# Optimization experiments

Measured on AMD Instinct MI355X. Metric: run time of the kernel, lower is better.

The kernel has to match this reference:

```python
import jax, jax.numpy as jnp
import numpy as np

H = 16      # numHeads (== numKeyValueHeads since keyValueHeadsPerHead=1)
D = 128     # headDim


def setup_inputs() -> dict:
    key = jax.random.key(0)
    k1, k2, k3 = jax.random.split(key, 3)
    B, S, dim = 2, 2048, 2048
    x = jax.random.normal(k1, (B, S, dim), dtype=jnp.float32)
    # qkvProj: Linear(dim -> (H + 2*H)*D) without bias; torch Linear weight is [out, in]
    Wqkv = jax.random.normal(k2, ((H + 2 * H) * D, dim), dtype=jnp.float32) * 0.02
    # outProj: Linear(H*D -> dim) without bias
    Wout = jax.random.normal(k3, (dim, H * D), dtype=jnp.float32) * 0.02
    return {"x": x, "Wqkv": Wqkv, "Wout": Wout}


def reference(x, Wqkv, Wout):
    B, S, _ = x.shape
    qkv = jnp.einsum('bsd,ed->bse', x, Wqkv)           # [B, S, 3*H*D]
    qkv = qkv.reshape(B, S, 3 * H, D)
    q = qkv[:, :, :H]                                  # [B, S, H, D]
    k = qkv[:, :, H:2 * H]                             # [B, S, H, D]
    v = qkv[:, :, 2 * H:]                              # [B, S, H, D]
    # explicit QK^T / sqrt(d), softmax in fp32, then @ V (keyValueHeadsPerHead=1
    # collapses the group axis, leaving standard per-head attention)
    logits = jnp.einsum('bqhd,bkhd->bhqk', q, k) * (D ** -0.5)
    w = jax.nn.softmax(logits.astype(jnp.float32), axis=-1).astype(logits.dtype)
    out = jnp.einsum('bhqk,bkhd->bqhd', w, v).reshape(B, S, H * D)
    return jnp.einsum('bse,de->bsd', out, Wout)        # outProj
```

## Files before the change

kernel.cpp:

```cpp
#include <hip/hip_runtime.h>

typedef __bf16 bf16x8 __attribute__((ext_vector_type(8)));
typedef _Float16 f16;
typedef f16 f16x8 __attribute__((ext_vector_type(8)));
typedef float f32x4 __attribute__((ext_vector_type(4)));
typedef unsigned short u16;
typedef u16 u16x4 __attribute__((ext_vector_type(4)));

__device__ __forceinline__ u16 f2bf(float f) {
  unsigned u = __builtin_bit_cast(unsigned, f);
  u += 0x7FFFu + ((u >> 16) & 1u);
  return (u16)(u >> 16);
}

#define GLDS16(g, l) __builtin_amdgcn_global_load_lds(                     \
    (const __attribute__((address_space(1))) unsigned int*)(g),            \
    (__attribute__((address_space(3))) unsigned int*)(l), 16, 0, 0)

__device__ __forceinline__ f32x4 mfma16(bf16x8 a, bf16x8 b, f32x4 c) {
  return __builtin_amdgcn_mfma_f32_16x16x32_bf16(a, b, c, 0, 0, 0);
}
__device__ __forceinline__ f32x4 mfma16h(f16x8 a, f16x8 b, f32x4 c) {
  return __builtin_amdgcn_mfma_f32_16x16x32_f16(a, b, c, 0, 0, 0);
}

__global__ void cvt_bf16(const float* __restrict__ src, u16* __restrict__ dst,
                         int n4, int n4s, float scale) {
  int idx = blockIdx.x * blockDim.x + threadIdx.x;
  int stride = gridDim.x * blockDim.x;
  for (int i = idx; i < n4; i += stride) {
    float4 v = ((const float4*)src)[i];
    float sc = (i < n4s) ? scale : 1.0f;
    u16x4 o = { f2bf(v.x * sc), f2bf(v.y * sc), f2bf(v.z * sc), f2bf(v.w * sc) };
    ((u16x4*)dst)[i] = o;
  }
}

template<int MODE>
__global__ __launch_bounds__(256, 3) void gemm_bt(
    const u16* __restrict__ A, const u16* __restrict__ B,
    void* __restrict__ C, u16* __restrict__ VT,
    int M, int N, int K) {
  __shared__ __align__(16) u16 As[2][128 * 32];
  __shared__ __align__(16) u16 Bs[2][128 * 32];
  const int t = threadIdx.x;
  const int lane = t & 63;
  const int w = t >> 6;
  const int wm = w >> 1, wn = w & 1;
  const int l15 = lane & 15, lg = lane >> 4;
  const int m0 = blockIdx.y * 128, n0 = blockIdx.x * 128;
  f32x4 acc[4][4] = {};

  const int srow = t >> 2;
  const int schunk = (t & 3) ^ ((srow >> 1) & 3);
  const u16* ga = A + (size_t)(m0 + srow) * K + schunk * 8;
  const u16* gb = B + (size_t)(n0 + srow) * K + schunk * 8;
  const size_t half = (size_t)64 * K;
  const int ro = l15 * 32 + ((lg ^ ((l15 >> 1) & 3)) * 8);

#define STG(kt, bf) do {                                                   \
    const int ko_ = (kt) * 32;                                             \
    GLDS16(ga + ko_,        &As[bf][0] + t * 8);                           \
    GLDS16(ga + half + ko_, &As[bf][2048] + t * 8);                        \
    GLDS16(gb + ko_,        &Bs[bf][0] + t * 8);                           \
    GLDS16(gb + half + ko_, &Bs[bf][2048] + t * 8);                        \
  } while (0)

#define BODY(bf) do {                                                      \
    const u16* la_ = &As[bf][0];                                           \
    const u16* lb_ = &Bs[bf][0];                                           \
    bf16x8 af[4], bfr[4];                                                  \
    _Pragma("unroll")                                                      \
    for (int i_ = 0; i_ < 4; ++i_)                                         \
      af[i_] = *(const bf16x8*)&la_[(wm * 64 + i_ * 16) * 32 + ro];        \
    _Pragma("unroll")                                                      \
    for (int i_ = 0; i_ < 4; ++i_)                                         \
      bfr[i_] = *(const bf16x8*)&lb_[(wn * 64 + i_ * 16) * 32 + ro];       \
    __builtin_amdgcn_s_setprio(1);                                         \
    _Pragma("unroll")                                                      \
    for (int i_ = 0; i_ < 4; ++i_)                                         \
      _Pragma("unroll")                                                    \
      for (int j_ = 0; j_ < 4; ++j_)                                       \
        acc[i_][j_] = mfma16(af[i_], bfr[j_], acc[i_][j_]);                \
    __builtin_amdgcn_s_setprio(0);                                         \
  } while (0)

  const int NT = K / 32;
  STG(0, 0);
#pragma unroll 1
  for (int T = 0; T < NT - 1; ++T) {
    STG(T + 1, (T + 1) & 1);
    asm volatile("s_waitcnt vmcnt(4)" ::: "memory");
    __builtin_amdgcn_sched_barrier(0);
    __builtin_amdgcn_s_barrier();
    __builtin_amdgcn_sched_barrier(0);
    BODY(T & 1);
    asm volatile("s_waitcnt lgkmcnt(0)" ::: "memory");
    __builtin_amdgcn_sched_barrier(0);
    __builtin_amdgcn_s_barrier();
    __builtin_amdgcn_sched_barrier(0);
  }
  asm volatile("s_waitcnt vmcnt(0)" ::: "memory");
  __builtin_amdgcn_sched_barrier(0);
  __builtin_amdgcn_s_barrier();
  __builtin_amdgcn_sched_barrier(0);
  BODY((NT - 1) & 1);
#undef STG
#undef BODY

  const int rbase = m0 + wm * 64 + (lg << 2);
  const int cbase = n0 + wn * 64 + l15;
#pragma unroll
  for (int i = 0; i < 4; ++i) {
#pragma unroll
    for (int j = 0; j < 4; ++j) {
      const int row0 = rbase + i * 16;
      const int col = cbase + j * 16;
      if (MODE == 0) {
        if (col < 4096) {
          u16* cq = (u16*)C;
#pragma unroll
          for (int jj = 0; jj < 4; ++jj)
            cq[(size_t)(row0 + jj) * 4096 + col] = f2bf(acc[i][j][jj]);
        } else {
          const int bb = row0 >> 11, s = row0 & 2047;
          auto h0 = __builtin_amdgcn_cvt_pkrtz(acc[i][j][0], acc[i][j][1]);
          auto h1 = __builtin_amdgcn_cvt_pkrtz(acc[i][j][2], acc[i][j][3]);
          uint2 pk;
          pk.x = __builtin_bit_cast(unsigned, h0);
          pk.y = __builtin_bit_cast(unsigned, h1);
          *(uint2*)&VT[(size_t)(bb * 2048 + (col - 4096)) * 2048 + s] = pk;
        }
      } else {
        float* cf = (float*)C;
#pragma unroll
        for (int jj = 0; jj < 4; ++jj)
          cf[(size_t)(row0 + jj) * N + col] = acc[i][j][jj];
      }
    }
  }
}

#define PSTRIDE 72
__global__ __launch_bounds__(512, 1) void attn_fwd(
    const u16* __restrict__ qk, const u16* __restrict__ vt, u16* __restrict__ aout) {
  __shared__ __align__(16) u16 Ks[2][64 * 128];
  __shared__ __align__(16) u16 Vs[2][128 * 64];
  __shared__ __align__(16) u16 Pl[8][32 * PSTRIDE];
  const int t = threadIdx.x, lane = t & 63, w = t >> 6;
  const int bh = blockIdx.x;
  const int b = bh >> 4, h = bh & 15;
  const int q0 = blockIdx.y * 256 + w * 32;
  const int l15 = lane & 15, lg = lane >> 4;

  const u16* qp = qk + (size_t)b * 2048 * 4096 + h * 128;
  const u16* kp = qp + 2048;
  const u16* vtp = vt + (size_t)(b * 16 + h) * 128 * 2048;
  u16* op = aout + (size_t)b * 2048 * 2048 + h * 128;

  int ksoff[2], vsoff[2];
#pragma unroll
  for (int rd = 0; rd < 2; ++rd) {
    const int r = rd * 32 + (t >> 4);
    const int c = (t & 15) ^ (r & 15);
    ksoff[rd] = r * 4096 + c * 8;
    const int rv = rd * 64 + (t >> 3);
    const int cv = (t & 7) ^ (rv & 7);
    vsoff[rd] = rv * 2048 + cv * 8;
  }

  bf16x8 qf[2][4];
#pragma unroll
  for (int mi = 0; mi < 2; ++mi)
#pragma unroll
    for (int kd = 0; kd < 4; ++kd)
      qf[mi][kd] = *(const bf16x8*)&qp[(size_t)(q0 + mi * 16 + l15) * 4096 + kd * 32 + lg * 8];

  f32x4 o[2][8] = {};
  f32x4 lacc[2] = {};
  const f16x8 onesf = {f16(1.f), f16(1.f), f16(1.f), f16(1.f),
                       f16(1.f), f16(1.f), f16(1.f), f16(1.f)};
  u16* pw = &Pl[w][0];

#pragma unroll
  for (int rd = 0; rd < 2; ++rd) {
    GLDS16(kp + ksoff[rd], &Ks[0][0] + rd * 4096 + t * 8);
    GLDS16(vtp + vsoff[rd], &Vs[0][0] + rd * 4096 + t * 8);
  }
  __syncthreads();

  auto tile = [&](const u16* ksb, const u16* vsb, u16* kpre, u16* vpre, int nextit) {
    if (nextit < 32) {
      const size_t kt1 = (size_t)nextit * 64;
#pragma unroll
      for (int rd = 0; rd < 2; ++rd) {
        GLDS16(kp + kt1 * 4096 + ksoff[rd], kpre + rd * 4096 + t * 8);
        GLDS16(vtp + kt1 + vsoff[rd], vpre + rd * 4096 + t * 8);
      }
    }
    f32x4 sf[2][4];
    __builtin_amdgcn_s_setprio(1);
#pragma unroll
    for (int ni = 0; ni < 4; ++ni) {
      const int r = ni * 16 + l15;
      bf16x8 kf[4];
#pragma unroll
      for (int kd = 0; kd < 4; ++kd)
        kf[kd] = *(const bf16x8*)&ksb[r * 128 + (((kd * 4 + lg) ^ l15) * 8)];
#pragma unroll
      for (int mi = 0; mi < 2; ++mi) {
        f32x4 s = {0.f, 0.f, 0.f, 0.f};
        s = mfma16(kf[0], qf[mi][0], s);
        s = mfma16(kf[1], qf[mi][1], s);
        s = mfma16(kf[2], qf[mi][2], s);
        s = mfma16(kf[3], qf[mi][3], s);
        sf[mi][ni] = s;
      }
    }
    __builtin_amdgcn_s_setprio(0);

#pragma unroll
    for (int mi = 0; mi < 2; ++mi)
#pragma unroll
      for (int ni = 0; ni < 4; ++ni) {
        float p0 = exp2f(sf[mi][ni][0]);
        float p1 = exp2f(sf[mi][ni][1]);
        float p2 = exp2f(sf[mi][ni][2]);
        float p3 = exp2f(sf[mi][ni][3]);
        auto h0 = __builtin_amdgcn_cvt_pkrtz(p0, p1);
        auto h1 = __builtin_amdgcn_cvt_pkrtz(p2, p3);
        uint2 wv;
        wv.x = __builtin_bit_cast(unsigned, h0);
        wv.y = __builtin_bit_cast(unsigned, h1);
        *(uint2*)&pw[(mi * 16 + l15) * PSTRIDE + ni * 16 + lg * 4] = wv;
      }

    f16x8 pa[2][2];
#pragma unroll
    for (int mi = 0; mi < 2; ++mi)
#pragma unroll
      for (int ks = 0; ks < 2; ++ks)
        pa[mi][ks] = *(const f16x8*)&pw[(mi * 16 + l15) * PSTRIDE + ks * 32 + lg * 8];
    __builtin_amdgcn_s_setprio(1);
#pragma unroll
    for (int mi = 0; mi < 2; ++mi) {
      lacc[mi] = mfma16h(pa[mi][0], onesf, lacc[mi]);
      lacc[mi] = mfma16h(pa[mi][1], onesf, lacc[mi]);
    }
#pragma unroll
    for (int n2 = 0; n2 < 8; ++n2) {
      const int r = n2 * 16 + l15;
      f16x8 vf0 = *(const f16x8*)&vsb[r * 64 + (((0 * 4 + lg) ^ (l15 & 7)) * 8)];
      f16x8 vf1 = *(const f16x8*)&vsb[r * 64 + (((1 * 4 + lg) ^ (l15 & 7)) * 8)];
#pragma unroll
      for (int mi = 0; mi < 2; ++mi) {
        o[mi][n2] = mfma16h(pa[mi][0], vf0, o[mi][n2]);
        o[mi][n2] = mfma16h(pa[mi][1], vf1, o[mi][n2]);
      }
    }
    __builtin_amdgcn_s_setprio(0);
    __syncthreads();
  };

#pragma unroll 1
  for (int it = 0; it < 32; it += 2) {
    tile(&Ks[0][0], &Vs[0][0], &Ks[1][0], &Vs[1][0], it + 1);
    tile(&Ks[1][0], &Vs[1][0], &Ks[0][0], &Vs[0][0], it + 2);
  }

#pragma unroll
  for (int mi = 0; mi < 2; ++mi)
#pragma unroll
    for (int j = 0; j < 4; ++j) {
      float inv = 1.f / lacc[mi][j];
#pragma unroll
      for (int n2 = 0; n2 < 8; ++n2)
        op[(size_t)(q0 + mi * 16 + lg * 4 + j) * 2048 + n2 * 16 + l15] =
            f2bf(o[mi][n2][j] * inv);
    }
}

extern "C" void kernel_launch(void* const* d_in, const int* in_sizes, int n_in,
                              void* d_out, int out_size, void* d_ws, size_t ws_size,
                              hipStream_t stream) {
  const float* x    = (const float*)d_in[0];
  const float* Wqkv = (const float*)d_in[1];
  const float* Wout = (const float*)d_in[2];
  float* out = (float*)d_out;

  u16* ws = (u16*)d_ws;
  u16* xb    = ws;
  u16* wqkvb = ws + 8388608;
  u16* woutb = ws + 20971520;
  u16* qkbuf = ws + 25165824;
  u16* vtbuf = ws + 41943040;
  u16* aout  = xb;

  const float qscale = 0.08838834764831845f * 1.4426950408889634f;

  cvt_bf16<<<2048, 256, 0, stream>>>(x,    xb,    8388608 / 4, 0, 1.0f);
  cvt_bf16<<<2048, 256, 0, stream>>>(Wqkv, wqkvb, 12582912 / 4, 4194304 / 4, qscale);
  cvt_bf16<<<1024, 256, 0, stream>>>(Wout, woutb, 4194304 / 4, 0, 1.0f);

  gemm_bt<0><<<dim3(48, 32), 256, 0, stream>>>(xb, wqkvb, (void*)qkbuf, vtbuf,
                                               4096, 6144, 2048);
  attn_fwd<<<dim3(32, 8, 1), 512, 0, stream>>>(qkbuf, vtbuf, aout);
  gemm_bt<1><<<dim3(16, 32), 256, 0, stream>>>(aout, woutb, (void*)out, nullptr,
                                               4096, 2048, 2048);
}
```

Baseline: 277.0 us.

## Add dedicated QKV GEMM kernel with 128x192 tiles and direct-register A loads; read V from global in attention

Replaces the generic QKV projection GEMM with a specialized kernel. It uses 128x192 output tiles, a 64-wide K step, and an XCD-aware block remapping. The A operand is loaded straight into registers from global memory with a one-step lookahead, and only B is staged through LDS. Separately, the attention kernel stops staging V^T through LDS and reads V fragments directly from global memory each tile. This frees LDS and drops the V staging loads, but V reads become uncoalesced global loads in the inner loop and may stall the MFMA pipeline.

```diff
diff --git a/kernel.cpp b/kernel.cpp
--- a/kernel.cpp
+++ b/kernel.cpp
@@ -36,11 +36,124 @@
   }
 }
 
-template<int MODE>
+__global__ __launch_bounds__(256, 2) void gemm1_qkv(
+    const u16* __restrict__ A, const u16* __restrict__ B,
+    u16* __restrict__ QK, u16* __restrict__ VT) {
+  __shared__ __align__(16) u16 LB[2][12288];
+  constexpr int K = 2048;
+  const int t = threadIdx.x, lane = t & 63, w = t >> 6;
+  const int wm = w >> 1, wn = w & 1;
+  const int l15 = lane & 15, lg = lane >> 4;
+  const int l7 = l15 & 7;
+
+  const int bid = blockIdx.x;
+  const int wg = (bid & 7) * 128 + (bid >> 3);
+  const int bx = wg & 31, by = wg >> 5;
+  const int m0 = by * 128, n0 = bx * 192;
+
+  const int srow = t >> 3;
+  const int schunk = (t & 7) ^ (srow & 7);
+  const u16* gb = B + (size_t)(n0 + srow) * K + schunk * 8;
+
+  const u16* gaf = A + (size_t)(m0 + wm * 64 + l15) * K + lg * 8;
+
+  f32x4 acc[4][6] = {};
+  bf16x8 aC[2][4], aN[2][4];
+
+#define STG_B6(kt, bfi) do {                                               \
+    GLDS16(gb + (kt) * 64 + (size_t)0 * 32 * K, &LB[bfi][0]     + t * 8);  \
+    GLDS16(gb + (kt) * 64 + (size_t)1 * 32 * K, &LB[bfi][2048]  + t * 8);  \
+    GLDS16(gb + (kt) * 64 + (size_t)2 * 32 * K, &LB[bfi][4096]  + t * 8);  \
+    GLDS16(gb + (kt) * 64 + (size_t)3 * 32 * K, &LB[bfi][6144]  + t * 8);  \
+    GLDS16(gb + (kt) * 64 + (size_t)4 * 32 * K, &LB[bfi][8192]  + t * 8);  \
+    GLDS16(gb + (kt) * 64 + (size_t)5 * 32 * K, &LB[bfi][10240] + t * 8);  \
+  } while (0)
+
+#define ITER(AC, AN, P, TT) do {                                           \
+    const bool st_ = (TT) < 31;                                            \
+    asm volatile("s_waitcnt lgkmcnt(0)" ::: "memory");                     \
+    __builtin_amdgcn_s_barrier();                                          \
+    if (st_) {                                                             \
+      _Pragma("unroll")                                                    \
+      for (int kk = 0; kk < 2; ++kk)                                       \
+        _Pragma("unroll")                                                  \
+        for (int i = 0; i < 4; ++i)                                        \
+          AN[kk][i] = *(const bf16x8*)&gaf[(size_t)i * 16 * K +            \
+                                           ((TT) + 1) * 64 + kk * 32];     \
+      STG_B6((TT) + 1, (P) ^ 1);                                           \
+      asm volatile("s_waitcnt vmcnt(14)" ::: "memory");                    \
+    } else {                                                               \
+      asm volatile("s_waitcnt vmcnt(0)" ::: "memory");                     \
+    }                                                                      \
+    __builtin_amdgcn_s_barrier();                                          \
+    const u16* lb_ = &LB[P][0];                                            \
+    bf16x8 bLo[2][3], bHi[2][3];                                           \
+    _Pragma("unroll")                                                      \
+    for (int kk = 0; kk < 2; ++kk) {                                       \
+      const int cp_ = ((kk * 4 + lg) ^ l7) * 8;                            \
+      _Pragma("unroll")                                                    \
+      for (int j = 0; j < 3; ++j) {                                        \
+        bLo[kk][j] = *(const bf16x8*)&lb_[(wn * 96 + j * 16 + l15) * 64 + cp_]; \
+        bHi[kk][j] = *(const bf16x8*)&lb_[(wn * 96 + 48 + j * 16 + l15) * 64 + cp_]; \
+      }                                                                    \
+    }                                                                      \
+    __builtin_amdgcn_s_setprio(1);                                         \
+    _Pragma("unroll")                                                      \
+    for (int i = 0; i < 4; ++i)                                            \
+      _Pragma("unroll")                                                    \
+      for (int j = 0; j < 6; ++j)                                          \
+        _Pragma("unroll")                                                  \
+        for (int kk = 0; kk < 2; ++kk)                                     \
+          acc[i][j] = mfma16(AC[kk][i],                                    \
+                             (j < 3 ? bLo[kk][j] : bHi[kk][j - 3]),        \
+                             acc[i][j]);                                   \
+    __builtin_amdgcn_s_setprio(0);                                         \
+  } while (0)
+
+#pragma unroll
+  for (int kk = 0; kk < 2; ++kk)
+#pragma unroll
+    for (int i = 0; i < 4; ++i)
+      aC[kk][i] = *(const bf16x8*)&gaf[(size_t)i * 16 * K + kk * 32];
+  STG_B6(0, 0);
+
+#pragma unroll 1
+  for (int T = 0; T < 32; T += 2) {
+    ITER(aC, aN, 0, T);
+    ITER(aN, aC, 1, T + 1);
+  }
+#undef STG_B6
+#undef ITER
+
+  const int rb = m0 + wm * 64 + lg * 4;
+  const int cb = n0 + wn * 96 + l15;
+#pragma unroll
+  for (int i = 0; i < 4; ++i) {
+#pragma unroll
+    for (int j = 0; j < 6; ++j) {
+      const int row0 = rb + i * 16;
+      const int col = cb + j * 16;
+      if (col < 4096) {
+#pragma unroll
+        for (int jj = 0; jj < 4; ++jj)
+          QK[(size_t)(row0 + jj) * 4096 + col] = f2bf(acc[i][j][jj]);
+      } else {
+        const int vcol = col - 4096;
+        const int bb = row0 >> 11, s = row0 & 2047;
+        auto h0 = __builtin_amdgcn_cvt_pkrtz(acc[i][j][0], acc[i][j][1]);
+        auto h1 = __builtin_amdgcn_cvt_pkrtz(acc[i][j][2], acc[i][j][3]);
+        uint2 pk;
+        pk.x = __builtin_bit_cast(unsigned, h0);
+        pk.y = __builtin_bit_cast(unsigned, h1);
+        *(uint2*)&VT[((size_t)bb * 2048 + vcol) * 2048 + s] = pk;
+      }
+    }
+  }
+}
+
 __global__ __launch_bounds__(256, 3) void gemm_bt(
     const u16* __restrict__ A, const u16* __restrict__ B,
-    void* __restrict__ C, u16* __restrict__ VT,
-    int M, int N, int K) {
+    float* __restrict__ C, int M, int N, int K) {
   __shared__ __align__(16) u16 As[2][128 * 32];
   __shared__ __align__(16) u16 Bs[2][128 * 32];
   const int t = threadIdx.x;
@@ -111,41 +224,21 @@
   const int rbase = m0 + wm * 64 + (lg << 2);
   const int cbase = n0 + wn * 64 + l15;
 #pragma unroll
-  for (int i = 0; i < 4; ++i) {
+  for (int i = 0; i < 4; ++i)
 #pragma unroll
     for (int j = 0; j < 4; ++j) {
       const int row0 = rbase + i * 16;
       const int col = cbase + j * 16;
-      if (MODE == 0) {
-        if (col < 4096) {
-          u16* cq = (u16*)C;
-#pragma unroll
-          for (int jj = 0; jj < 4; ++jj)
-            cq[(size_t)(row0 + jj) * 4096 + col] = f2bf(acc[i][j][jj]);
-        } else {
-          const int bb = row0 >> 11, s = row0 & 2047;
-          auto h0 = __builtin_amdgcn_cvt_pkrtz(acc[i][j][0], acc[i][j][1]);
-          auto h1 = __builtin_amdgcn_cvt_pkrtz(acc[i][j][2], acc[i][j][3]);
-          uint2 pk;
-          pk.x = __builtin_bit_cast(unsigned, h0);
-          pk.y = __builtin_bit_cast(unsigned, h1);
-          *(uint2*)&VT[(size_t)(bb * 2048 + (col - 4096)) * 2048 + s] = pk;
-        }
-      } else {
-        float* cf = (float*)C;
-#pragma unroll
-        for (int jj = 0; jj < 4; ++jj)
-          cf[(size_t)(row0 + jj) * N + col] = acc[i][j][jj];
-      }
-    }
-  }
+#pragma unroll
+      for (int jj = 0; jj < 4; ++jj)
+        C[(size_t)(row0 + jj) * N + col] = acc[i][j][jj];
+    }
 }
 
 #define PSTRIDE 72
 __global__ __launch_bounds__(512, 1) void attn_fwd(
     const u16* __restrict__ qk, const u16* __restrict__ vt, u16* __restrict__ aout) {
   __shared__ __align__(16) u16 Ks[2][64 * 128];
-  __shared__ __align__(16) u16 Vs[2][128 * 64];
   __shared__ __align__(16) u16 Pl[8][32 * PSTRIDE];
   const int t = threadIdx.x, lane = t & 63, w = t >> 6;
   const int bh = blockIdx.x;
@@ -158,15 +251,12 @@
   const u16* vtp = vt + (size_t)(b * 16 + h) * 128 * 2048;
   u16* op = aout + (size_t)b * 2048 * 2048 + h * 128;
 
-  int ksoff[2], vsoff[2];
+  int ksoff[2];
 #pragma unroll
   for (int rd = 0; rd < 2; ++rd) {
     const int r = rd * 32 + (t >> 4);
     const int c = (t & 15) ^ (r & 15);
     ksoff[rd] = r * 4096 + c * 8;
-    const int rv = rd * 64 + (t >> 3);
-    const int cv = (t & 7) ^ (rv & 7);
-    vsoff[rd] = rv * 2048 + cv * 8;
   }
 
   bf16x8 qf[2][4];
@@ -183,21 +273,18 @@
   u16* pw = &Pl[w][0];
 
 #pragma unroll
-  for (int rd = 0; rd < 2; ++rd) {
+  for (int rd = 0; rd < 2; ++rd)
     GLDS16(kp + ksoff[rd], &Ks[0][0] + rd * 4096 + t * 8);
-    GLDS16(vtp + vsoff[rd], &Vs[0][0] + rd * 4096 + t * 8);
-  }
   __syncthreads();
 
-  auto tile = [&](const u16* ksb, const u16* vsb, u16* kpre, u16* vpre, int nextit) {
-    if (nextit < 32) {
-      const size_t kt1 = (size_t)nextit * 64;
-#pragma unroll
-      for (int rd = 0; rd < 2; ++rd) {
+  auto tile = [&](const u16* ksb, u16* kpre, int it) {
+    if (it + 1 < 32) {
+      const size_t kt1 = (size_t)(it + 1) * 64;
+#pragma unroll
+      for (int rd = 0; rd < 2; ++rd)
         GLDS16(kp + kt1 * 4096 + ksoff[rd], kpre + rd * 4096 + t * 8);
-        GLDS16(vtp + kt1 + vsoff[rd], vpre + rd * 4096 + t * 8);
-      }
-    }
+    }
+    const int kt = it * 64;
     f32x4 sf[2][4];
     __builtin_amdgcn_s_setprio(1);
 #pragma unroll
@@ -249,9 +336,9 @@
     }
 #pragma unroll
     for (int n2 = 0; n2 < 8; ++n2) {
-      const int r = n2 * 16 + l15;
-      f16x8 vf0 = *(const f16x8*)&vsb[r * 64 + (((0 * 4 + lg) ^ (l15 & 7)) * 8)];
-      f16x8 vf1 = *(const f16x8*)&vsb[r * 64 + (((1 * 4 + lg) ^ (l15 & 7)) * 8)];
+      const u16* vr = &vtp[(size_t)(n2 * 16 + l15) * 2048 + kt + lg * 8];
+      f16x8 vf0 = *(const f16x8*)(vr);
+      f16x8 vf1 = *(const f16x8*)(vr + 32);
 #pragma unroll
       for (int mi = 0; mi < 2; ++mi) {
         o[mi][n2] = mfma16h(pa[mi][0], vf0, o[mi][n2]);
@@ -264,8 +351,8 @@
 
 #pragma unroll 1
   for (int it = 0; it < 32; it += 2) {
-    tile(&Ks[0][0], &Vs[0][0], &Ks[1][0], &Vs[1][0], it + 1);
-    tile(&Ks[1][0], &Vs[1][0], &Ks[0][0], &Vs[0][0], it + 2);
+    tile(&Ks[0][0], &Ks[1][0], it);
+    tile(&Ks[1][0], &Ks[0][0], it + 1);
   }
 
 #pragma unroll
@@ -302,9 +389,7 @@
   cvt_bf16<<<2048, 256, 0, stream>>>(Wqkv, wqkvb, 12582912 / 4, 4194304 / 4, qscale);
   cvt_bf16<<<1024, 256, 0, stream>>>(Wout, woutb, 4194304 / 4, 0, 1.0f);
 
-  gemm_bt<0><<<dim3(48, 32), 256, 0, stream>>>(xb, wqkvb, (void*)qkbuf, vtbuf,
-                                               4096, 6144, 2048);
+  gemm1_qkv<<<1024, 256, 0, stream>>>(xb, wqkvb, qkbuf, vtbuf);
   attn_fwd<<<dim3(32, 8, 1), 512, 0, stream>>>(qkbuf, vtbuf, aout);
-  gemm_bt<1><<<dim3(16, 32), 256, 0, stream>>>(aout, woutb, (void*)out, nullptr,
-                                               4096, 2048, 2048);
-}
+  gemm_bt<<<dim3(16, 32), 256, 0, stream>>>(aout, woutb, out, 4096, 2048, 2048);
+}
```

Result: slower. 407.2 us (+47.0%).
